# Optimization experiments

Hardware: AMD Instinct MI355X
Metric: run time of the kernel (lower is better)

## Reference

```python
import jax, jax.numpy as jnp
import numpy as np

N_NODES = 100000


def _sage_conv(x, src, dst, Wl, b, Wr):
    """PyG SAGEConv with mean aggregation: lin_l(mean_{j->i} x_j) + lin_r(x_i)."""
    msg = x[src]  # [E, d] gather of source-node features
    s = jax.ops.segment_sum(msg, dst, num_segments=N_NODES)  # [N, d]
    deg = jax.ops.segment_sum(jnp.ones_like(dst, dtype=x.dtype), dst,
                              num_segments=N_NODES)  # [N]
    mean = s / jnp.maximum(deg, 1.0)[:, None]  # nodes with no in-edges -> 0
    return mean @ Wl.T + b + x @ Wr.T


def setup_inputs() -> dict:
    key = jax.random.key(0)
    ks = jax.random.split(key, 12)
    in_f, h_f, out_f = 64, 64, 32
    E_half = 800000
    x = jax.random.normal(ks[0], (N_NODES, in_f), dtype=jnp.float32)
    edge_index1 = jax.random.randint(ks[1], (2, E_half), 0, N_NODES, dtype=jnp.int64)
    edge_weight1 = jax.random.uniform(ks[2], (E_half,), dtype=jnp.float32)
    edge_index2 = jax.random.randint(ks[3], (2, E_half), 0, N_NODES, dtype=jnp.int64)
    edge_weight2 = jax.random.uniform(ks[4], (E_half,), dtype=jnp.float32)
    s1 = 1.0 / np.sqrt(in_f)
    s2 = 1.0 / np.sqrt(h_f)
    W1l = jax.random.uniform(ks[5], (h_f, in_f), minval=-s1, maxval=s1, dtype=jnp.float32)
    b1 = jax.random.uniform(ks[6], (h_f,), minval=-s1, maxval=s1, dtype=jnp.float32)
    W1r = jax.random.uniform(ks[7], (h_f, in_f), minval=-s1, maxval=s1, dtype=jnp.float32)
    W2l = jax.random.uniform(ks[8], (out_f, h_f), minval=-s2, maxval=s2, dtype=jnp.float32)
    b2 = jax.random.uniform(ks[9], (out_f,), minval=-s2, maxval=s2, dtype=jnp.float32)
    W2r = jax.random.uniform(ks[10], (out_f, h_f), minval=-s2, maxval=s2, dtype=jnp.float32)
    return {"x": x, "edge_index1": edge_index1, "edge_weight1": edge_weight1,
            "edge_index2": edge_index2, "edge_weight2": edge_weight2,
            "W1l": W1l, "b1": b1, "W1r": W1r, "W2l": W2l, "b2": b2, "W2r": W2r}


def reference(x, edge_index1, edge_weight1, edge_index2, edge_weight2,
              W1l, b1, W1r, W2l, b2, W2r):
    # concat adjacency lists (edge_weight is concatenated but unused by SAGEConv)
    edge_index = jnp.concatenate([edge_index1, edge_index2], axis=-1)
    _edge_weight = jnp.concatenate([edge_weight1, edge_weight2], axis=-1)  # unused
    src, dst = edge_index[0], edge_index[1]
    # F.dropout with training=False -> identity (eval-mode reference)
    h = _sage_conv(x, src, dst, W1l, b1, W1r)
    h = jax.nn.relu(h)
    out = _sage_conv(h, src, dst, W2l, b2, W2r)
    return out
```

## Files before the change

kernel.cpp:

```cpp
#include <hip/hip_runtime.h>


constexpr int N_NODES = 100000;
constexpr int E_HALF  = 800000;
constexpr int E_TOT   = 2 * E_HALF;
constexpr int CAP     = 64;
constexpr int OVF_CAP = 4096;
constexpr int NB      = 200;
constexpr int NPB     = 500;
constexpr int BCAP    = 12288;
constexpr int EPB_A   = 2048;
constexpr int EPT_A   = EPB_A / 256;

typedef short  s16x8 __attribute__((ext_vector_type(8)));
typedef float  f32x4 __attribute__((ext_vector_type(4)));
typedef unsigned short u16;

__device__ inline float bf(u16 u) { return __uint_as_float(((unsigned)u) << 16); }
__device__ inline u16 f2bf(float v) {
    unsigned b = __float_as_uint(v);
    b += 0x7FFFu + ((b >> 16) & 1u);
    return (u16)(b >> 16);
}

__global__ __launch_bounds__(256) void binA_kernel(
    const int* __restrict__ ei1, const int* __restrict__ ei2,
    uint2* __restrict__ barr, int* __restrict__ bcur,
    int* __restrict__ ovfA_cnt, int* __restrict__ ovfA)
{
    __shared__ int   hist[NB], base[NB], cur[NB], lofs[NB];
    __shared__ int   scan[256];
    __shared__ int   aux[EPB_A];
    __shared__ uint2 staged[EPB_A];
    int tid = threadIdx.x;
    for (int t = tid; t < NB; t += 256) { hist[t] = 0; cur[t] = 0; }
    __syncthreads();

    int e0 = blockIdx.x * EPB_A;
    uint2 myE[EPT_A];
    int   myB[EPT_A];
    #pragma unroll
    for (int k = 0; k < EPT_A; k++) {
        int e = e0 + k * 256 + tid;
        myB[k] = -1;
        if (e < E_TOT) {
            const int* ei = (e < E_HALF) ? ei1 : ei2;
            int ee = (e < E_HALF) ? e : e - E_HALF;
            int dst = ei[E_HALF + ee];
            int src = ei[ee];
            myE[k] = make_uint2((unsigned)src, (unsigned)dst);
            myB[k] = dst / NPB;
            atomicAdd(&hist[myB[k]], 1);
        }
    }
    __syncthreads();

    int v = (tid < NB) ? hist[tid] : 0;
    scan[tid] = v;
    __syncthreads();
    #pragma unroll
    for (int off = 1; off < 256; off <<= 1) {
        int u = (tid >= off) ? scan[tid - off] : 0;
        __syncthreads();
        scan[tid] += u;
        __syncthreads();
    }
    if (tid < NB) lofs[tid] = scan[tid] - v;
    if (tid < NB) base[tid] = atomicAdd(&bcur[tid], hist[tid]);
    __syncthreads();

    #pragma unroll
    for (int k = 0; k < EPT_A; k++) {
        int b = myB[k];
        if (b < 0) continue;
        int rank = atomicAdd(&cur[b], 1);
        int p    = lofs[b] + rank;
        int gpos = base[b] + rank;
        if (gpos < BCAP) {
            staged[p] = myE[k];
            aux[p]    = b * BCAP + gpos;
        } else {
            aux[p] = -1;
            int o = atomicAdd(ovfA_cnt, 1);
            if (o < OVF_CAP) {
                ovfA[2 * o] = (int)myE[k].x; ovfA[2 * o + 1] = (int)myE[k].y;
            }
        }
    }
    __syncthreads();

    int tot = scan[255];
    for (int i = tid; i < tot; i += 256) {
        int a = aux[i];
        if (a >= 0) barr[a] = staged[i];
    }
}

__global__ __launch_bounds__(1024) void binB_kernel(
    const uint2* __restrict__ barr, const int* __restrict__ bcur,
    int* __restrict__ cnt, int* __restrict__ slots,
    int* __restrict__ ovfB_cnt, int* __restrict__ ovfB)
{
    __shared__ int lcnt[NPB];
    int tid = threadIdx.x, b = blockIdx.x;
    for (int t = tid; t < NPB; t += 1024) lcnt[t] = 0;
    __syncthreads();
    int nE = bcur[b]; if (nE > BCAP) nE = BCAP;
    int dbase = b * NPB;
    for (int i = tid; i < nE; i += 1024) {
        uint2 e = barr[b * BCAP + i];
        int dst = (int)e.y;
        int pos = atomicAdd(&lcnt[dst - dbase], 1);
        if (pos < CAP) {
            slots[dst * CAP + pos] = (int)e.x;
        } else {
            int o = atomicAdd(ovfB_cnt, 1);
            if (o < OVF_CAP) { ovfB[2 * o] = (int)e.x; ovfB[2 * o + 1] = dst; }
        }
    }
    __syncthreads();
    for (int t = tid; t < NPB; t += 1024) {
        int n = dbase + t;
        if (n < N_NODES) cnt[n] = lcnt[t];
    }
}

__global__ __launch_bounds__(256) void ovf_fix_kernel(
    const int* __restrict__ ovfA_cnt, const int* __restrict__ ovfA,
    int* __restrict__ cnt)
{
    int n = *ovfA_cnt; if (n > OVF_CAP) n = OVF_CAP;
    int t = blockIdx.x * 256 + threadIdx.x;
    if (t < n) atomicAdd(&cnt[ovfA[2 * t + 1]], 1);
}

__global__ __launch_bounds__(256) void prep_kernel(
    const float* __restrict__ x, u16* __restrict__ xb,
    const float* __restrict__ W1l, const float* __restrict__ W1r,
    const float* __restrict__ W2l, const float* __restrict__ W2r,
    short* __restrict__ B1hi, short* __restrict__ B1lo,
    short* __restrict__ B2hi, short* __restrict__ B2lo)
{
    int blk = blockIdx.x;
    if (blk < 6250) {
        int i = blk * 256 + threadIdx.x;
        float4 v = ((const float4*)x)[i];
        ushort4 rr;
        rr.x = f2bf(v.x); rr.y = f2bf(v.y); rr.z = f2bf(v.z); rr.w = f2bf(v.w);
        ((ushort4*)xb)[i] = rr;
        return;
    }
    int i = (blk - 6250) * 256 + threadIdx.x;
    float v; short* ph; short* pl; int idx;
    if (i < 64 * 128) {
        int o = i >> 7, k = i & 127;
        v = (k < 64) ? W1l[o * 64 + k] : W1r[o * 64 + (k - 64)];
        ph = B1hi; pl = B1lo; idx = i;
    } else {
        int j = i - 64 * 128;
        int o = j >> 6, k = j & 63;
        v = (o < 32) ? W2l[o * 64 + k] : W2r[(o - 32) * 64 + k];
        ph = B2hi; pl = B2lo; idx = j;
    }
    unsigned b  = __float_as_uint(v);
    float    hf = __uint_as_float(b & 0xFFFF0000u);
    float    r  = v - hf;
    ph[idx] = (short)(b >> 16);
    pl[idx] = (short)(__float_as_uint(r) >> 16);
}

__global__ __launch_bounds__(256) void gather_mean_kernel(
    const u16*  __restrict__ xb,
    const int*  __restrict__ cnt,
    const int*  __restrict__ slots,
    float*      __restrict__ m)
{
    int node = blockIdx.x * 4 + (threadIdx.x >> 6);
    int lane = threadIdx.x & 63;
    int r    = lane >> 4;
    int c    = lane & 15;
    if (node >= N_NODES) return;
    int cdeg = cnt[node];
    int cc   = cdeg < CAP ? cdeg : CAP;
    int slotv = (lane < cc) ? slots[node * CAP + lane] : 0;
    float a0 = 0.f, a1 = 0.f, a2 = 0.f, a3 = 0.f;
    float b0 = 0.f, b1 = 0.f, b2 = 0.f, b3 = 0.f;
    float c0 = 0.f, c1 = 0.f, c2 = 0.f, c3 = 0.f;
    float d0 = 0.f, d1 = 0.f, d2 = 0.f, d3 = 0.f;
    for (int i = 0; i < cc; i += 16) {
        int iA = i + r, iB = i + 4 + r, iC = i + 8 + r, iD = i + 12 + r;
        int sA = __shfl(slotv, iA & 63);
        int sB = __shfl(slotv, iB & 63);
        int sC = __shfl(slotv, iC & 63);
        int sD = __shfl(slotv, iD & 63);
        ushort4 vA = make_ushort4(0,0,0,0), vB = make_ushort4(0,0,0,0);
        ushort4 vC = make_ushort4(0,0,0,0), vD = make_ushort4(0,0,0,0);
        if (iA < cc) vA = *(const ushort4*)&xb[sA * 64 + c * 4];
        if (iB < cc) vB = *(const ushort4*)&xb[sB * 64 + c * 4];
        if (iC < cc) vC = *(const ushort4*)&xb[sC * 64 + c * 4];
        if (iD < cc) vD = *(const ushort4*)&xb[sD * 64 + c * 4];
        a0 += bf(vA.x); a1 += bf(vA.y); a2 += bf(vA.z); a3 += bf(vA.w);
        b0 += bf(vB.x); b1 += bf(vB.y); b2 += bf(vB.z); b3 += bf(vB.w);
        c0 += bf(vC.x); c1 += bf(vC.y); c2 += bf(vC.z); c3 += bf(vC.w);
        d0 += bf(vD.x); d1 += bf(vD.y); d2 += bf(vD.z); d3 += bf(vD.w);
    }
    a0 += b0 + c0 + d0; a1 += b1 + c1 + d1;
    a2 += b2 + c2 + d2; a3 += b3 + c3 + d3;
    a0 += __shfl_xor(a0, 16); a0 += __shfl_xor(a0, 32);
    a1 += __shfl_xor(a1, 16); a1 += __shfl_xor(a1, 32);
    a2 += __shfl_xor(a2, 16); a2 += __shfl_xor(a2, 32);
    a3 += __shfl_xor(a3, 16); a3 += __shfl_xor(a3, 32);
    if (r == 0) {
        float rd = 1.0f / fmaxf((float)cdeg, 1.0f);
        *(float4*)&m[node * 64 + c * 4] =
            make_float4(a0 * rd, a1 * rd, a2 * rd, a3 * rd);
    }
}

__global__ __launch_bounds__(256) void gather_mean32_kernel(
    const u16*  __restrict__ y2b,
    const float* __restrict__ z,
    const int*  __restrict__ cnt,
    const int*  __restrict__ slots,
    float*      __restrict__ out)
{
    int node = blockIdx.x * 4 + (threadIdx.x >> 6);
    int lane = threadIdx.x & 63;
    int r    = lane >> 3;
    int c    = lane & 7;
    if (node >= N_NODES) return;
    int cdeg = cnt[node];
    int cc   = cdeg < CAP ? cdeg : CAP;
    int slotv = (lane < cc) ? slots[node * CAP + lane] : 0;
    float a0 = 0.f, a1 = 0.f, a2 = 0.f, a3 = 0.f;
    float b0 = 0.f, b1 = 0.f, b2 = 0.f, b3 = 0.f;
    float c0 = 0.f, c1 = 0.f, c2 = 0.f, c3 = 0.f;
    float d0 = 0.f, d1 = 0.f, d2 = 0.f, d3 = 0.f;
    for (int i = 0; i < cc; i += 32) {
        int iA = i + r, iB = i + 8 + r, iC = i + 16 + r, iD = i + 24 + r;
        int sA = __shfl(slotv, iA & 63);
        int sB = __shfl(slotv, iB & 63);
        int sC = __shfl(slotv, iC & 63);
        int sD = __shfl(slotv, iD & 63);
        ushort4 vA = make_ushort4(0,0,0,0), vB = make_ushort4(0,0,0,0);
        ushort4 vC = make_ushort4(0,0,0,0), vD = make_ushort4(0,0,0,0);
        if (iA < cc) vA = *(const ushort4*)&y2b[sA * 32 + c * 4];
        if (iB < cc) vB = *(const ushort4*)&y2b[sB * 32 + c * 4];
        if (iC < cc) vC = *(const ushort4*)&y2b[sC * 32 + c * 4];
        if (iD < cc) vD = *(const ushort4*)&y2b[sD * 32 + c * 4];
        a0 += bf(vA.x); a1 += bf(vA.y); a2 += bf(vA.z); a3 += bf(vA.w);
        b0 += bf(vB.x); b1 += bf(vB.y); b2 += bf(vB.z); b3 += bf(vB.w);
        c0 += bf(vC.x); c1 += bf(vC.y); c2 += bf(vC.z); c3 += bf(vC.w);
        d0 += bf(vD.x); d1 += bf(vD.y); d2 += bf(vD.z); d3 += bf(vD.w);
    }
    a0 += b0 + c0 + d0; a1 += b1 + c1 + d1;
    a2 += b2 + c2 + d2; a3 += b3 + c3 + d3;
    a0 += __shfl_xor(a0, 8); a0 += __shfl_xor(a0, 16); a0 += __shfl_xor(a0, 32);
    a1 += __shfl_xor(a1, 8); a1 += __shfl_xor(a1, 16); a1 += __shfl_xor(a1, 32);
    a2 += __shfl_xor(a2, 8); a2 += __shfl_xor(a2, 16); a2 += __shfl_xor(a2, 32);
    a3 += __shfl_xor(a3, 8); a3 += __shfl_xor(a3, 16); a3 += __shfl_xor(a3, 32);
    if (r == 0) {
        float rd = 1.0f / fmaxf((float)cdeg, 1.0f);
        float4 zz = *(const float4*)&z[node * 32 + c * 4];
        *(float4*)&out[node * 32 + c * 4] = make_float4(
            a0 * rd + zz.x, a1 * rd + zz.y, a2 * rd + zz.z, a3 * rd + zz.w);
    }
}

__global__ __launch_bounds__(256) void ovf_apply_kernel(
    const float* __restrict__ feat, const int* __restrict__ cnt,
    const int* __restrict__ ovfA_cnt, const int* __restrict__ ovfA,
    const int* __restrict__ ovfB_cnt, const int* __restrict__ ovfB,
    float* __restrict__ m)
{
    int nA = *ovfA_cnt; if (nA > OVF_CAP) nA = OVF_CAP;
    int nB = *ovfB_cnt; if (nB > OVF_CAP) nB = OVF_CAP;
    int total = (nA + nB) * 64;
    for (int t = blockIdx.x * 256 + threadIdx.x; t < total; t += gridDim.x * 256) {
        int o = t >> 6, f = t & 63;
        const int* L = (o < nA) ? &ovfA[2 * o] : &ovfB[2 * (o - nA)];
        int src = L[0], dst = L[1];
        float rd = 1.0f / fmaxf((float)cnt[dst], 1.0f);
        atomicAdd(&m[dst * 64 + f], feat[src * 64 + f] * rd);
    }
}

__global__ __launch_bounds__(256) void ovf_apply32_kernel(
    const u16* __restrict__ y2b, const int* __restrict__ cnt,
    const int* __restrict__ ovfA_cnt, const int* __restrict__ ovfA,
    const int* __restrict__ ovfB_cnt, const int* __restrict__ ovfB,
    float* __restrict__ out)
{
    int nA = *ovfA_cnt; if (nA > OVF_CAP) nA = OVF_CAP;
    int nB = *ovfB_cnt; if (nB > OVF_CAP) nB = OVF_CAP;
    int total = (nA + nB) * 32;
    for (int t = blockIdx.x * 256 + threadIdx.x; t < total; t += gridDim.x * 256) {
        int o = t >> 5, f = t & 31;
        const int* L = (o < nA) ? &ovfA[2 * o] : &ovfB[2 * (o - nA)];
        int src = L[0], dst = L[1];
        float rd = 1.0f / fmaxf((float)cnt[dst], 1.0f);
        atomicAdd(&out[dst * 32 + f], bf(y2b[src * 32 + f]) * rd);
    }
}

__device__ inline void split8(float4 v0, float4 v1, s16x8& hi, s16x8& lo) {
    float vs[8] = {v0.x, v0.y, v0.z, v0.w, v1.x, v1.y, v1.z, v1.w};
    s16x8 h, l;
    #pragma unroll
    for (int j = 0; j < 8; j++) {
        unsigned b  = __float_as_uint(vs[j]);
        float    hf = __uint_as_float(b & 0xFFFF0000u);
        float    r  = vs[j] - hf;
        h[j] = (short)(b >> 16);
        l[j] = (short)(__float_as_uint(r) >> 16);
    }
    hi = h; lo = l;
}

template <int MT>
__global__ __launch_bounds__(256) void gemm1_kernel(
    const float* __restrict__ Am, const float* __restrict__ Ax,
    const short* __restrict__ Bhi, const short* __restrict__ Blo,
    const float* __restrict__ bias, u16* __restrict__ hb)
{
    int wave = (blockIdx.x * 256 + threadIdx.x) >> 6;
    int lane = threadIdx.x & 63;
    int m0   = wave * (MT * 16);
    if (m0 >= N_NODES) return;
    int quad = lane >> 4, l16 = lane & 15;

    f32x4 acc[MT][4];
    #pragma unroll
    for (int mt = 0; mt < MT; mt++)
        #pragma unroll
        for (int nt = 0; nt < 4; nt++) acc[mt][nt] = (f32x4)0.0f;

    #pragma unroll
    for (int half = 0; half < 2; half++) {
        const float* src = half ? Ax : Am;
        #pragma unroll
        for (int sub = 0; sub < 2; sub++) {
            int kf = sub * 32 + quad * 8;
            int kc = half * 64 + sub * 32 + quad * 8;
            s16x8 ahi[MT], alo[MT];
            #pragma unroll
            for (int mt = 0; mt < MT; mt++) {
                int row = m0 + mt * 16 + l16;
                row = row < N_NODES ? row : N_NODES - 1;
                const float4* p = (const float4*)&src[row * 64 + kf];
                split8(p[0], p[1], ahi[mt], alo[mt]);
            }
            #pragma unroll
            for (int nt = 0; nt < 4; nt++) {
                int n = nt * 16 + l16;
                s16x8 bh = *(const s16x8*)&Bhi[n * 128 + kc];
                s16x8 bl = *(const s16x8*)&Blo[n * 128 + kc];
                #pragma unroll
                for (int mt = 0; mt < MT; mt++) {
                    acc[mt][nt] = __builtin_amdgcn_mfma_f32_16x16x32_bf16(ahi[mt], bh, acc[mt][nt], 0, 0, 0);
                    acc[mt][nt] = __builtin_amdgcn_mfma_f32_16x16x32_bf16(alo[mt], bh, acc[mt][nt], 0, 0, 0);
                    acc[mt][nt] = __builtin_amdgcn_mfma_f32_16x16x32_bf16(ahi[mt], bl, acc[mt][nt], 0, 0, 0);
                    acc[mt][nt] = __builtin_amdgcn_mfma_f32_16x16x32_bf16(alo[mt], bl, acc[mt][nt], 0, 0, 0);
                }
            }
        }
    }
    #pragma unroll
    for (int nt = 0; nt < 4; nt++) {
        float bv = bias[nt * 16 + l16];
        #pragma unroll
        for (int mt = 0; mt < MT; mt++)
            #pragma unroll
            for (int r = 0; r < 4; r++) {
                int row = m0 + mt * 16 + quad * 4 + r;
                if (row < N_NODES)
                    hb[row * 64 + nt * 16 + l16] =
                        f2bf(fmaxf(acc[mt][nt][r] + bv, 0.0f));
            }
    }
}

template <int MT>
__global__ __launch_bounds__(256) void gemm2_kernel(
    const u16* __restrict__ hb,
    const short* __restrict__ Bhi, const short* __restrict__ Blo,
    const float* __restrict__ b2,
    u16* __restrict__ y2b, float* __restrict__ z)
{
    int wave = (blockIdx.x * 256 + threadIdx.x) >> 6;
    int lane = threadIdx.x & 63;
    int m0   = wave * (MT * 16);
    if (m0 >= N_NODES) return;
    int quad = lane >> 4, l16 = lane & 15;

    f32x4 acc[MT][4];
    #pragma unroll
    for (int mt = 0; mt < MT; mt++)
        #pragma unroll
        for (int nt = 0; nt < 4; nt++) acc[mt][nt] = (f32x4)0.0f;

    #pragma unroll
    for (int sub = 0; sub < 2; sub++) {
        int kf = sub * 32 + quad * 8;
        s16x8 a[MT];
        #pragma unroll
        for (int mt = 0; mt < MT; mt++) {
            int row = m0 + mt * 16 + l16;
            row = row < N_NODES ? row : N_NODES - 1;
            a[mt] = *(const s16x8*)&hb[row * 64 + kf];
        }
        #pragma unroll
        for (int nt = 0; nt < 4; nt++) {
            int n = nt * 16 + l16;
            s16x8 bh = *(const s16x8*)&Bhi[n * 64 + kf];
            s16x8 bl = *(const s16x8*)&Blo[n * 64 + kf];
            #pragma unroll
            for (int mt = 0; mt < MT; mt++) {
                acc[mt][nt] = __builtin_amdgcn_mfma_f32_16x16x32_bf16(a[mt], bh, acc[mt][nt], 0, 0, 0);
                acc[mt][nt] = __builtin_amdgcn_mfma_f32_16x16x32_bf16(a[mt], bl, acc[mt][nt], 0, 0, 0);
            }
        }
    }
    #pragma unroll
    for (int nt = 0; nt < 4; nt++) {
        bool  isz = nt >= 2;
        int   col = (isz ? nt - 2 : nt) * 16 + l16;
        float bv  = isz ? b2[col] : 0.0f;
        #pragma unroll
        for (int mt = 0; mt < MT; mt++)
            #pragma unroll
            for (int r = 0; r < 4; r++) {
                int row = m0 + mt * 16 + quad * 4 + r;
                if (row < N_NODES) {
                    float v = acc[mt][nt][r] + bv;
                    if (isz) z[row * 32 + col] = v;
                    else     y2b[row * 32 + col] = f2bf(v);
                }
            }
    }
}

extern "C" void kernel_launch(void* const* d_in, const int* in_sizes, int n_in,
                              void* d_out, int out_size, void* d_ws, size_t ws_size,
                              hipStream_t stream) {
    const float* x   = (const float*)d_in[0];
    const int*   ei1 = (const int*)d_in[1];
    const int*   ei2 = (const int*)d_in[3];
    const float* W1l = (const float*)d_in[5];
    const float* b1  = (const float*)d_in[6];
    const float* W1r = (const float*)d_in[7];
    const float* W2l = (const float*)d_in[8];
    const float* b2  = (const float*)d_in[9];
    const float* W2r = (const float*)d_in[10];
    float* out = (float*)d_out;

    const size_t off_cnt   = 0;
    const size_t off_misc  = 400128;
    const size_t off_ovfAc = off_misc + 0;
    const size_t off_ovfBc = off_misc + 4;
    const size_t off_bcur  = off_misc + 256;
    const size_t off_ovfA  = off_misc + 1280;
    const size_t off_ovfB  = off_misc + 1280 + 8 * OVF_CAP;
    const size_t off_slots = 467200;
    const size_t off_m     = off_slots + (size_t)N_NODES * CAP * 4;
    const size_t off_h     = off_m + (size_t)N_NODES * 64 * 4;
    const size_t off_hb    = off_h + (size_t)N_NODES * 64 * 2;
    const size_t off_B1hi  = off_h + (size_t)N_NODES * 64 * 4;
    const size_t off_B1lo  = off_B1hi + 64 * 128 * 2;
    const size_t off_B2hi  = off_B1lo + 64 * 128 * 2;
    const size_t off_B2lo  = off_B2hi + 64 * 64 * 2;

    char*  ws     = (char*)d_ws;
    int*   cnt    = (int*)(ws + off_cnt);
    int*   ovfA_c = (int*)(ws + off_ovfAc);
    int*   ovfB_c = (int*)(ws + off_ovfBc);
    int*   bcur   = (int*)(ws + off_bcur);
    int*   ovfA   = (int*)(ws + off_ovfA);
    int*   ovfB   = (int*)(ws + off_ovfB);
    int*   slots  = (int*)(ws + off_slots);
    uint2* barr   = (uint2*)(ws + off_m);
    float* m      = (float*)(ws + off_m);
    u16*   xb     = (u16*)(ws + off_h);
    u16*   hb     = (u16*)(ws + off_hb);
    float* z      = (float*)(ws + off_m);
    u16*   y2b    = (u16*)(ws + off_m + (size_t)N_NODES * 32 * 4);
    short* B1hi   = (short*)(ws + off_B1hi);
    short* B1lo   = (short*)(ws + off_B1lo);
    short* B2hi   = (short*)(ws + off_B2hi);
    short* B2lo   = (short*)(ws + off_B2lo);

    hipMemsetAsync(ws + off_misc, 0, off_slots - off_misc, stream);

    prep_kernel<<<6250 + 48, 256, 0, stream>>>(
        x, xb, W1l, W1r, W2l, W2r, B1hi, B1lo, B2hi, B2lo);

    binA_kernel<<<(E_TOT + EPB_A - 1) / EPB_A, 256, 0, stream>>>(
        ei1, ei2, barr, bcur, ovfA_c, ovfA);
    binB_kernel<<<NB, 1024, 0, stream>>>(barr, bcur, cnt, slots, ovfB_c, ovfB);
    ovf_fix_kernel<<<OVF_CAP / 256, 256, 0, stream>>>(ovfA_c, ovfA, cnt);

    gather_mean_kernel<<<N_NODES / 4, 256, 0, stream>>>(xb, cnt, slots, m);
    ovf_apply_kernel<<<16, 256, 0, stream>>>(
        x, cnt, ovfA_c, ovfA, ovfB_c, ovfB, m);
    {
        int waves = (N_NODES + 31) / 32;
        gemm1_kernel<2><<<(waves + 3) / 4, 256, 0, stream>>>(
            m, x, B1hi, B1lo, b1, hb);
    }

    {
        int waves = (N_NODES + 63) / 64;
        gemm2_kernel<4><<<(waves + 3) / 4, 256, 0, stream>>>(
            hb, B2hi, B2lo, b2, y2b, z);
    }
    gather_mean32_kernel<<<N_NODES / 4, 256, 0, stream>>>(y2b, z, cnt, slots, out);
    ovf_apply32_kernel<<<16, 256, 0, stream>>>(
        y2b, cnt, ovfA_c, ovfA, ovfB_c, ovfB, out);
}
```

Measured before the change: 246.8 us.

## Fuse layer-1 gather-mean into GEMM1 and fold overflow handling into binning/gather

The layer-1 neighbour mean is now computed per wave straight into LDS and consumed by the MFMA GEMM, so the fp32 mean buffer no longer makes a round trip through global memory. The ovf_fix and both ovf_apply launches are removed. Bin-A overflow edges are merged into slots inside binB, and bin-B overflow is applied inside the gather kernels by linearly scanning the overflow list. The memset is replaced by a zeroing block inside prep_kernel. This cuts several launches and memory traffic, at the cost of per-wave serial overflow scans and larger LDS use that may lower occupancy. The layer-1 overflow path now adds bf16 xb features where the old path used fp32 x, which slightly changes precision.

```diff
diff --git a/kernel.cpp b/kernel.cpp
--- a/kernel.cpp
+++ b/kernel.cpp
@@ -21,6 +21,12 @@
     unsigned b = __float_as_uint(v);
     b += 0x7FFFu + ((b >> 16) & 1u);
     return (u16)(b >> 16);
+}
+__device__ inline void acc4(float* s, uint2 v) {
+    s[0] += __uint_as_float(v.x << 16);
+    s[1] += __uint_as_float(v.x & 0xFFFF0000u);
+    s[2] += __uint_as_float(v.y << 16);
+    s[3] += __uint_as_float(v.y & 0xFFFF0000u);
 }
 
 __global__ __launch_bounds__(256) void binA_kernel(
@@ -98,6 +104,7 @@
 
 __global__ __launch_bounds__(1024) void binB_kernel(
     const uint2* __restrict__ barr, const int* __restrict__ bcur,
+    const int* __restrict__ ovfA_cnt, const int* __restrict__ ovfA,
     int* __restrict__ cnt, int* __restrict__ slots,
     int* __restrict__ ovfB_cnt, int* __restrict__ ovfB)
 {
@@ -119,19 +126,24 @@
         }
     }
     __syncthreads();
+    int nOA = *ovfA_cnt; if (nOA > OVF_CAP) nOA = OVF_CAP;
+    for (int t = tid; t < nOA; t += 1024) {
+        int src = ovfA[2 * t], dst = ovfA[2 * t + 1];
+        if (dst >= dbase && dst < dbase + NPB) {
+            int pos = atomicAdd(&lcnt[dst - dbase], 1);
+            if (pos < CAP) {
+                slots[dst * CAP + pos] = src;
+            } else {
+                int o = atomicAdd(ovfB_cnt, 1);
+                if (o < OVF_CAP) { ovfB[2 * o] = src; ovfB[2 * o + 1] = dst; }
+            }
+        }
+    }
+    __syncthreads();
     for (int t = tid; t < NPB; t += 1024) {
         int n = dbase + t;
         if (n < N_NODES) cnt[n] = lcnt[t];
     }
-}
-
-__global__ __launch_bounds__(256) void ovf_fix_kernel(
-    const int* __restrict__ ovfA_cnt, const int* __restrict__ ovfA,
-    int* __restrict__ cnt)
-{
-    int n = *ovfA_cnt; if (n > OVF_CAP) n = OVF_CAP;
-    int t = blockIdx.x * 256 + threadIdx.x;
-    if (t < n) atomicAdd(&cnt[ovfA[2 * t + 1]], 1);
 }
 
 __global__ __launch_bounds__(256) void prep_kernel(
@@ -139,9 +151,14 @@
     const float* __restrict__ W1l, const float* __restrict__ W1r,
     const float* __restrict__ W2l, const float* __restrict__ W2r,
     short* __restrict__ B1hi, short* __restrict__ B1lo,
-    short* __restrict__ B2hi, short* __restrict__ B2lo)
+    short* __restrict__ B2hi, short* __restrict__ B2lo,
+    int* __restrict__ zinit)
 {
     int blk = blockIdx.x;
+    if (blk == 6298) {
+        for (int t = threadIdx.x; t < 320; t += 256) zinit[t] = 0;
+        return;
+    }
     if (blk < 6250) {
         int i = blk * 256 + threadIdx.x;
         float4 v = ((const float4*)x)[i];
@@ -169,140 +186,6 @@
     pl[idx] = (short)(__float_as_uint(r) >> 16);
 }
 
-__global__ __launch_bounds__(256) void gather_mean_kernel(
-    const u16*  __restrict__ xb,
-    const int*  __restrict__ cnt,
-    const int*  __restrict__ slots,
-    float*      __restrict__ m)
-{
-    int node = blockIdx.x * 4 + (threadIdx.x >> 6);
-    int lane = threadIdx.x & 63;
-    int r    = lane >> 4;
-    int c    = lane & 15;
-    if (node >= N_NODES) return;
-    int cdeg = cnt[node];
-    int cc   = cdeg < CAP ? cdeg : CAP;
-    int slotv = (lane < cc) ? slots[node * CAP + lane] : 0;
-    float a0 = 0.f, a1 = 0.f, a2 = 0.f, a3 = 0.f;
-    float b0 = 0.f, b1 = 0.f, b2 = 0.f, b3 = 0.f;
-    float c0 = 0.f, c1 = 0.f, c2 = 0.f, c3 = 0.f;
-    float d0 = 0.f, d1 = 0.f, d2 = 0.f, d3 = 0.f;
-    for (int i = 0; i < cc; i += 16) {
-        int iA = i + r, iB = i + 4 + r, iC = i + 8 + r, iD = i + 12 + r;
-        int sA = __shfl(slotv, iA & 63);
-        int sB = __shfl(slotv, iB & 63);
-        int sC = __shfl(slotv, iC & 63);
-        int sD = __shfl(slotv, iD & 63);
-        ushort4 vA = make_ushort4(0,0,0,0), vB = make_ushort4(0,0,0,0);
-        ushort4 vC = make_ushort4(0,0,0,0), vD = make_ushort4(0,0,0,0);
-        if (iA < cc) vA = *(const ushort4*)&xb[sA * 64 + c * 4];
-        if (iB < cc) vB = *(const ushort4*)&xb[sB * 64 + c * 4];
-        if (iC < cc) vC = *(const ushort4*)&xb[sC * 64 + c * 4];
-        if (iD < cc) vD = *(const ushort4*)&xb[sD * 64 + c * 4];
-        a0 += bf(vA.x); a1 += bf(vA.y); a2 += bf(vA.z); a3 += bf(vA.w);
-        b0 += bf(vB.x); b1 += bf(vB.y); b2 += bf(vB.z); b3 += bf(vB.w);
-        c0 += bf(vC.x); c1 += bf(vC.y); c2 += bf(vC.z); c3 += bf(vC.w);
-        d0 += bf(vD.x); d1 += bf(vD.y); d2 += bf(vD.z); d3 += bf(vD.w);
-    }
-    a0 += b0 + c0 + d0; a1 += b1 + c1 + d1;
-    a2 += b2 + c2 + d2; a3 += b3 + c3 + d3;
-    a0 += __shfl_xor(a0, 16); a0 += __shfl_xor(a0, 32);
-    a1 += __shfl_xor(a1, 16); a1 += __shfl_xor(a1, 32);
-    a2 += __shfl_xor(a2, 16); a2 += __shfl_xor(a2, 32);
-    a3 += __shfl_xor(a3, 16); a3 += __shfl_xor(a3, 32);
-    if (r == 0) {
-        float rd = 1.0f / fmaxf((float)cdeg, 1.0f);
-        *(float4*)&m[node * 64 + c * 4] =
-            make_float4(a0 * rd, a1 * rd, a2 * rd, a3 * rd);
-    }
-}
-
-__global__ __launch_bounds__(256) void gather_mean32_kernel(
-    const u16*  __restrict__ y2b,
-    const float* __restrict__ z,
-    const int*  __restrict__ cnt,
-    const int*  __restrict__ slots,
-    float*      __restrict__ out)
-{
-    int node = blockIdx.x * 4 + (threadIdx.x >> 6);
-    int lane = threadIdx.x & 63;
-    int r    = lane >> 3;
-    int c    = lane & 7;
-    if (node >= N_NODES) return;
-    int cdeg = cnt[node];
-    int cc   = cdeg < CAP ? cdeg : CAP;
-    int slotv = (lane < cc) ? slots[node * CAP + lane] : 0;
-    float a0 = 0.f, a1 = 0.f, a2 = 0.f, a3 = 0.f;
-    float b0 = 0.f, b1 = 0.f, b2 = 0.f, b3 = 0.f;
-    float c0 = 0.f, c1 = 0.f, c2 = 0.f, c3 = 0.f;
-    float d0 = 0.f, d1 = 0.f, d2 = 0.f, d3 = 0.f;
-    for (int i = 0; i < cc; i += 32) {
-        int iA = i + r, iB = i + 8 + r, iC = i + 16 + r, iD = i + 24 + r;
-        int sA = __shfl(slotv, iA & 63);
-        int sB = __shfl(slotv, iB & 63);
-        int sC = __shfl(slotv, iC & 63);
-        int sD = __shfl(slotv, iD & 63);
-        ushort4 vA = make_ushort4(0,0,0,0), vB = make_ushort4(0,0,0,0);
-        ushort4 vC = make_ushort4(0,0,0,0), vD = make_ushort4(0,0,0,0);
-        if (iA < cc) vA = *(const ushort4*)&y2b[sA * 32 + c * 4];
-        if (iB < cc) vB = *(const ushort4*)&y2b[sB * 32 + c * 4];
-        if (iC < cc) vC = *(const ushort4*)&y2b[sC * 32 + c * 4];
-        if (iD < cc) vD = *(const ushort4*)&y2b[sD * 32 + c * 4];
-        a0 += bf(vA.x); a1 += bf(vA.y); a2 += bf(vA.z); a3 += bf(vA.w);
-        b0 += bf(vB.x); b1 += bf(vB.y); b2 += bf(vB.z); b3 += bf(vB.w);
-        c0 += bf(vC.x); c1 += bf(vC.y); c2 += bf(vC.z); c3 += bf(vC.w);
-        d0 += bf(vD.x); d1 += bf(vD.y); d2 += bf(vD.z); d3 += bf(vD.w);
-    }
-    a0 += b0 + c0 + d0; a1 += b1 + c1 + d1;
-    a2 += b2 + c2 + d2; a3 += b3 + c3 + d3;
-    a0 += __shfl_xor(a0, 8); a0 += __shfl_xor(a0, 16); a0 += __shfl_xor(a0, 32);
-    a1 += __shfl_xor(a1, 8); a1 += __shfl_xor(a1, 16); a1 += __shfl_xor(a1, 32);
-    a2 += __shfl_xor(a2, 8); a2 += __shfl_xor(a2, 16); a2 += __shfl_xor(a2, 32);
-    a3 += __shfl_xor(a3, 8); a3 += __shfl_xor(a3, 16); a3 += __shfl_xor(a3, 32);
-    if (r == 0) {
-        float rd = 1.0f / fmaxf((float)cdeg, 1.0f);
-        float4 zz = *(const float4*)&z[node * 32 + c * 4];
-        *(float4*)&out[node * 32 + c * 4] = make_float4(
-            a0 * rd + zz.x, a1 * rd + zz.y, a2 * rd + zz.z, a3 * rd + zz.w);
-    }
-}
-
-__global__ __launch_bounds__(256) void ovf_apply_kernel(
-    const float* __restrict__ feat, const int* __restrict__ cnt,
-    const int* __restrict__ ovfA_cnt, const int* __restrict__ ovfA,
-    const int* __restrict__ ovfB_cnt, const int* __restrict__ ovfB,
-    float* __restrict__ m)
-{
-    int nA = *ovfA_cnt; if (nA > OVF_CAP) nA = OVF_CAP;
-    int nB = *ovfB_cnt; if (nB > OVF_CAP) nB = OVF_CAP;
-    int total = (nA + nB) * 64;
-    for (int t = blockIdx.x * 256 + threadIdx.x; t < total; t += gridDim.x * 256) {
-        int o = t >> 6, f = t & 63;
-        const int* L = (o < nA) ? &ovfA[2 * o] : &ovfB[2 * (o - nA)];
-        int src = L[0], dst = L[1];
-        float rd = 1.0f / fmaxf((float)cnt[dst], 1.0f);
-        atomicAdd(&m[dst * 64 + f], feat[src * 64 + f] * rd);
-    }
-}
-
-__global__ __launch_bounds__(256) void ovf_apply32_kernel(
-    const u16* __restrict__ y2b, const int* __restrict__ cnt,
-    const int* __restrict__ ovfA_cnt, const int* __restrict__ ovfA,
-    const int* __restrict__ ovfB_cnt, const int* __restrict__ ovfB,
-    float* __restrict__ out)
-{
-    int nA = *ovfA_cnt; if (nA > OVF_CAP) nA = OVF_CAP;
-    int nB = *ovfB_cnt; if (nB > OVF_CAP) nB = OVF_CAP;
-    int total = (nA + nB) * 32;
-    for (int t = blockIdx.x * 256 + threadIdx.x; t < total; t += gridDim.x * 256) {
-        int o = t >> 5, f = t & 31;
-        const int* L = (o < nA) ? &ovfA[2 * o] : &ovfB[2 * (o - nA)];
-        int src = L[0], dst = L[1];
-        float rd = 1.0f / fmaxf((float)cnt[dst], 1.0f);
-        atomicAdd(&out[dst * 32 + f], bf(y2b[src * 32 + f]) * rd);
-    }
-}
-
 __device__ inline void split8(float4 v0, float4 v1, s16x8& hi, s16x8& lo) {
     float vs[8] = {v0.x, v0.y, v0.z, v0.w, v1.x, v1.y, v1.z, v1.w};
     s16x8 h, l;
@@ -318,16 +201,103 @@
 }
 
 template <int MT>
-__global__ __launch_bounds__(256) void gemm1_kernel(
-    const float* __restrict__ Am, const float* __restrict__ Ax,
+__global__ __launch_bounds__(256) void gather_gemm1_kernel(
+    const u16*  __restrict__ xb,
+    const float* __restrict__ x,
+    const int*  __restrict__ cnt,
+    const int*  __restrict__ slots,
+    const int*  __restrict__ ovfB_cnt, const int* __restrict__ ovfB,
     const short* __restrict__ Bhi, const short* __restrict__ Blo,
     const float* __restrict__ bias, u16* __restrict__ hb)
 {
-    int wave = (blockIdx.x * 256 + threadIdx.x) >> 6;
-    int lane = threadIdx.x & 63;
-    int m0   = wave * (MT * 16);
-    if (m0 >= N_NODES) return;
-    int quad = lane >> 4, l16 = lane & 15;
+    constexpr int RPW = MT * 16;
+    __shared__ float ldsA[4][RPW][66];
+    const int widx = threadIdx.x >> 6;
+    const int lane = threadIdx.x & 63;
+    const int m0   = (blockIdx.x * 4 + widx) * RPW;
+    const int r = lane >> 4;
+    const int c = lane & 15;
+
+    int pdA, pdB, psvA, psvB;
+    {
+        int nA = m0, nB = m0 + 1;
+        pdA  = (nA < N_NODES) ? cnt[nA] : 0;
+        pdB  = (nB < N_NODES) ? cnt[nB] : 0;
+        psvA = (nA < N_NODES) ? slots[nA * CAP + lane] : 0;
+        psvB = (nB < N_NODES) ? slots[nB * CAP + lane] : 0;
+    }
+    #pragma unroll 1
+    for (int j = 0; j < RPW; j += 2) {
+        const int dA = pdA, dB = pdB;
+        const int rsvA = psvA, rsvB = psvB;
+        if (j + 2 < RPW) {
+            int nA = m0 + j + 2, nB = m0 + j + 3;
+            pdA  = (nA < N_NODES) ? cnt[nA] : 0;
+            pdB  = (nB < N_NODES) ? cnt[nB] : 0;
+            psvA = (nA < N_NODES) ? slots[nA * CAP + lane] : 0;
+            psvB = (nB < N_NODES) ? slots[nB * CAP + lane] : 0;
+        }
+        const int cA = dA < CAP ? dA : CAP;
+        const int cB = dB < CAP ? dB : CAP;
+        const int svA = (lane < cA) ? rsvA : 0;
+        const int svB = (lane < cB) ? rsvB : 0;
+        float sA[16], sB[16];
+        #pragma unroll
+        for (int k = 0; k < 16; k++) { sA[k] = 0.f; sB[k] = 0.f; }
+        const int cM = cA > cB ? cA : cB;
+        for (int i = 0; i < cM; i += 16) {
+            const int i0 = i + r, i1 = i + 4 + r, i2 = i + 8 + r, i3 = i + 12 + r;
+            int tA0 = __shfl(svA, i0), tA1 = __shfl(svA, i1),
+                tA2 = __shfl(svA, i2), tA3 = __shfl(svA, i3);
+            int tB0 = __shfl(svB, i0), tB1 = __shfl(svB, i1),
+                tB2 = __shfl(svB, i2), tB3 = __shfl(svB, i3);
+            uint2 vA0 = make_uint2(0u, 0u), vA1 = vA0, vA2 = vA0, vA3 = vA0;
+            uint2 vB0 = vA0, vB1 = vA0, vB2 = vA0, vB3 = vA0;
+            if (i0 < cA) vA0 = *(const uint2*)&xb[tA0 * 64 + c * 4];
+            if (i1 < cA) vA1 = *(const uint2*)&xb[tA1 * 64 + c * 4];
+            if (i2 < cA) vA2 = *(const uint2*)&xb[tA2 * 64 + c * 4];
+            if (i3 < cA) vA3 = *(const uint2*)&xb[tA3 * 64 + c * 4];
+            if (i0 < cB) vB0 = *(const uint2*)&xb[tB0 * 64 + c * 4];
+            if (i1 < cB) vB1 = *(const uint2*)&xb[tB1 * 64 + c * 4];
+            if (i2 < cB) vB2 = *(const uint2*)&xb[tB2 * 64 + c * 4];
+            if (i3 < cB) vB3 = *(const uint2*)&xb[tB3 * 64 + c * 4];
+            acc4(&sA[0], vA0); acc4(&sA[4], vA1);
+            acc4(&sA[8], vA2); acc4(&sA[12], vA3);
+            acc4(&sB[0], vB0); acc4(&sB[4], vB1);
+            acc4(&sB[8], vB2); acc4(&sB[12], vB3);
+        }
+        #pragma unroll
+        for (int k = 0; k < 4; k++) {
+            float fA = sA[k] + sA[k + 4] + sA[k + 8] + sA[k + 12];
+            float fB = sB[k] + sB[k + 4] + sB[k + 8] + sB[k + 12];
+            fA += __shfl_xor(fA, 16); fA += __shfl_xor(fA, 32);
+            fB += __shfl_xor(fB, 16); fB += __shfl_xor(fB, 32);
+            sA[k] = fA; sB[k] = fB;
+        }
+        if (r == 0) {
+            const float rdA = 1.0f / fmaxf((float)dA, 1.0f);
+            const float rdB = 1.0f / fmaxf((float)dB, 1.0f);
+            float2* pA = (float2*)&ldsA[widx][j][c * 4];
+            float2* pB = (float2*)&ldsA[widx][j + 1][c * 4];
+            pA[0] = make_float2(sA[0] * rdA, sA[1] * rdA);
+            pA[1] = make_float2(sA[2] * rdA, sA[3] * rdA);
+            pB[0] = make_float2(sB[0] * rdB, sB[1] * rdB);
+            pB[1] = make_float2(sB[2] * rdB, sB[3] * rdB);
+        }
+    }
+    __syncthreads();
+
+    {
+        int nOv = *ovfB_cnt; if (nOv > OVF_CAP) nOv = OVF_CAP;
+        for (int t = 0; t < nOv; ++t) {
+            int src = ovfB[2 * t], dst = ovfB[2 * t + 1];
+            if (dst >= m0 && dst < m0 + RPW && dst < N_NODES) {
+                float rd = 1.0f / fmaxf((float)cnt[dst], 1.0f);
+                ldsA[widx][dst - m0][lane] += bf(xb[src * 64 + lane]) * rd;
+            }
+        }
+    }
+    __syncthreads();
 
     f32x4 acc[MT][4];
     #pragma unroll
@@ -337,22 +307,29 @@
 
     #pragma unroll
     for (int half = 0; half < 2; half++) {
-        const float* src = half ? Ax : Am;
         #pragma unroll
         for (int sub = 0; sub < 2; sub++) {
-            int kf = sub * 32 + quad * 8;
-            int kc = half * 64 + sub * 32 + quad * 8;
+            const int kf = sub * 32 + r * 8;
+            const int kc = half * 64 + kf;
             s16x8 ahi[MT], alo[MT];
             #pragma unroll
             for (int mt = 0; mt < MT; mt++) {
-                int row = m0 + mt * 16 + l16;
-                row = row < N_NODES ? row : N_NODES - 1;
-                const float4* p = (const float4*)&src[row * 64 + kf];
-                split8(p[0], p[1], ahi[mt], alo[mt]);
+                if (half == 0) {
+                    const float2* p = (const float2*)&ldsA[widx][mt * 16 + c][kf];
+                    float2 q0 = p[0], q1 = p[1], q2 = p[2], q3 = p[3];
+                    split8(make_float4(q0.x, q0.y, q1.x, q1.y),
+                           make_float4(q2.x, q2.y, q3.x, q3.y),
+                           ahi[mt], alo[mt]);
+                } else {
+                    int row = m0 + mt * 16 + c;
+                    row = row < N_NODES ? row : N_NODES - 1;
+                    const float4* p = (const float4*)&x[row * 64 + kf];
+                    split8(p[0], p[1], ahi[mt], alo[mt]);
+                }
             }
             #pragma unroll
             for (int nt = 0; nt < 4; nt++) {
-                int n = nt * 16 + l16;
+                const int n = nt * 16 + c;
                 s16x8 bh = *(const s16x8*)&Bhi[n * 128 + kc];
                 s16x8 bl = *(const s16x8*)&Blo[n * 128 + kc];
                 #pragma unroll
@@ -367,15 +344,15 @@
     }
     #pragma unroll
     for (int nt = 0; nt < 4; nt++) {
-        float bv = bias[nt * 16 + l16];
+        float bv = bias[nt * 16 + c];
         #pragma unroll
         for (int mt = 0; mt < MT; mt++)
             #pragma unroll
-            for (int r = 0; r < 4; r++) {
-                int row = m0 + mt * 16 + quad * 4 + r;
+            for (int rr = 0; rr < 4; rr++) {
+                int row = m0 + mt * 16 + r * 4 + rr;
                 if (row < N_NODES)
-                    hb[row * 64 + nt * 16 + l16] =
-                        f2bf(fmaxf(acc[mt][nt][r] + bv, 0.0f));
+                    hb[row * 64 + nt * 16 + c] =
+                        f2bf(fmaxf(acc[mt][nt][rr] + bv, 0.0f));
             }
     }
 }
@@ -437,6 +414,62 @@
                     else     y2b[row * 32 + col] = f2bf(v);
                 }
             }
+    }
+}
+
+__global__ __launch_bounds__(256) void gather_mean32_kernel(
+    const u16*  __restrict__ y2b,
+    const float* __restrict__ z,
+    const int*  __restrict__ cnt,
+    const int*  __restrict__ slots,
+    const int*  __restrict__ ovfB_cnt, const int* __restrict__ ovfB,
+    float*      __restrict__ out)
+{
+    int node = blockIdx.x * 4 + (threadIdx.x >> 6);
+    int lane = threadIdx.x & 63;
+    int r    = lane >> 3;
+    int c    = lane & 7;
+    if (node >= N_NODES) return;
+    int nOv = *ovfB_cnt; if (nOv > OVF_CAP) nOv = OVF_CAP;
+    int cdeg = cnt[node];
+    int cc   = cdeg < CAP ? cdeg : CAP;
+    int slotv = (lane < cc) ? slots[node * CAP + lane] : 0;
+    float s[16];
+    #pragma unroll
+    for (int k = 0; k < 16; k++) s[k] = 0.f;
+    for (int i = 0; i < cc; i += 32) {
+        int i0 = i + r, i1 = i + 8 + r, i2 = i + 16 + r, i3 = i + 24 + r;
+        int t0 = __shfl(slotv, i0), t1 = __shfl(slotv, i1),
+            t2 = __shfl(slotv, i2), t3 = __shfl(slotv, i3);
+        uint2 v0 = make_uint2(0u, 0u), v1 = v0, v2 = v0, v3 = v0;
+        if (i0 < cc) v0 = *(const uint2*)&y2b[t0 * 32 + c * 4];
+        if (i1 < cc) v1 = *(const uint2*)&y2b[t1 * 32 + c * 4];
+        if (i2 < cc) v2 = *(const uint2*)&y2b[t2 * 32 + c * 4];
+        if (i3 < cc) v3 = *(const uint2*)&y2b[t3 * 32 + c * 4];
+        acc4(&s[0], v0); acc4(&s[4], v1); acc4(&s[8], v2); acc4(&s[12], v3);
+    }
+    #pragma unroll
+    for (int k = 0; k < 4; k++) {
+        float f = s[k] + s[k + 4] + s[k + 8] + s[k + 12];
+        f += __shfl_xor(f, 8); f += __shfl_xor(f, 16); f += __shfl_xor(f, 32);
+        s[k] = f;
+    }
+    for (int t = 0; t < nOv; ++t) {
+        int src = ovfB[2 * t], dst = ovfB[2 * t + 1];
+        if (dst == node) {
+            uint2 v = *(const uint2*)&y2b[src * 32 + c * 4];
+            s[0] += __uint_as_float(v.x << 16);
+            s[1] += __uint_as_float(v.x & 0xFFFF0000u);
+            s[2] += __uint_as_float(v.y << 16);
+            s[3] += __uint_as_float(v.y & 0xFFFF0000u);
+        }
+    }
+    if (r == 0) {
+        float rd = 1.0f / fmaxf((float)cdeg, 1.0f);
+        float4 zz = *(const float4*)&z[node * 32 + c * 4];
+        *(float4*)&out[node * 32 + c * 4] = make_float4(
+            s[0] * rd + zz.x, s[1] * rd + zz.y,
+            s[2] * rd + zz.z, s[3] * rd + zz.w);
     }
 }
 
@@ -454,7 +487,6 @@
     const float* W2r = (const float*)d_in[10];
     float* out = (float*)d_out;
 
-    const size_t off_cnt   = 0;
     const size_t off_misc  = 400128;
     const size_t off_ovfAc = off_misc + 0;
     const size_t off_ovfBc = off_misc + 4;
@@ -471,7 +503,7 @@
     const size_t off_B2lo  = off_B2hi + 64 * 64 * 2;
 
     char*  ws     = (char*)d_ws;
-    int*   cnt    = (int*)(ws + off_cnt);
+    int*   cnt    = (int*)(ws + 0);
     int*   ovfA_c = (int*)(ws + off_ovfAc);
     int*   ovfB_c = (int*)(ws + off_ovfBc);
     int*   bcur   = (int*)(ws + off_bcur);
@@ -479,7 +511,6 @@
     int*   ovfB   = (int*)(ws + off_ovfB);
     int*   slots  = (int*)(ws + off_slots);
     uint2* barr   = (uint2*)(ws + off_m);
-    float* m      = (float*)(ws + off_m);
     u16*   xb     = (u16*)(ws + off_h);
     u16*   hb     = (u16*)(ws + off_hb);
     float* z      = (float*)(ws + off_m);
@@ -489,23 +520,20 @@
     short* B2hi   = (short*)(ws + off_B2hi);
     short* B2lo   = (short*)(ws + off_B2lo);
 
-    hipMemsetAsync(ws + off_misc, 0, off_slots - off_misc, stream);
-
-    prep_kernel<<<6250 + 48, 256, 0, stream>>>(
-        x, xb, W1l, W1r, W2l, W2r, B1hi, B1lo, B2hi, B2lo);
+    prep_kernel<<<6250 + 48 + 1, 256, 0, stream>>>(
+        x, xb, W1l, W1r, W2l, W2r, B1hi, B1lo, B2hi, B2lo,
+        (int*)(ws + off_misc));
 
     binA_kernel<<<(E_TOT + EPB_A - 1) / EPB_A, 256, 0, stream>>>(
         ei1, ei2, barr, bcur, ovfA_c, ovfA);
-    binB_kernel<<<NB, 1024, 0, stream>>>(barr, bcur, cnt, slots, ovfB_c, ovfB);
-    ovf_fix_kernel<<<OVF_CAP / 256, 256, 0, stream>>>(ovfA_c, ovfA, cnt);
-
-    gather_mean_kernel<<<N_NODES / 4, 256, 0, stream>>>(xb, cnt, slots, m);
-    ovf_apply_kernel<<<16, 256, 0, stream>>>(
-        x, cnt, ovfA_c, ovfA, ovfB_c, ovfB, m);
+    binB_kernel<<<NB, 1024, 0, stream>>>(
+        barr, bcur, ovfA_c, ovfA, cnt, slots, ovfB_c, ovfB);
+
     {
-        int waves = (N_NODES + 31) / 32;
-        gemm1_kernel<2><<<(waves + 3) / 4, 256, 0, stream>>>(
-            m, x, B1hi, B1lo, b1, hb);
+        int waves  = (N_NODES + 31) / 32;
+        int blocks = (waves + 3) / 4;
+        gather_gemm1_kernel<2><<<blocks, 256, 0, stream>>>(
+            xb, x, cnt, slots, ovfB_c, ovfB, B1hi, B1lo, b1, hb);
     }
 
     {
@@ -513,7 +541,6 @@
         gemm2_kernel<4><<<(waves + 3) / 4, 256, 0, stream>>>(
             hb, B2hi, B2lo, b2, y2b, z);
     }
-    gather_mean32_kernel<<<N_NODES / 4, 256, 0, stream>>>(y2b, z, cnt, slots, out);
-    ovf_apply32_kernel<<<16, 256, 0, stream>>>(
-        y2b, cnt, ovfA_c, ovfA, ovfB_c, ovfB, out);
-}
+    gather_mean32_kernel<<<N_NODES / 4, 256, 0, stream>>>(
+        y2b, z, cnt, slots, ovfB_c, ovfB, out);
+}
```

Measured after the change: 236.9 us. -4.0%, faster.
